# Kernel tuning notes

Hardware: AMD Instinct MI355X
Metric: run time of the kernel (lower is better)

Reference implementation:

```python
import jax, jax.numpy as jnp
import numpy as np

N_NODES = 50000
N_EDGES = 400000
D_IN = 256
D_OUT = 256
DROPOUT_P = 0.1


def setup_inputs() -> dict:
    key = jax.random.key(0)
    k_feat, k_w, k_src, k_dst = jax.random.split(key, 4)
    feat = jax.random.normal(k_feat, (N_NODES, D_IN), dtype=jnp.float32)
    # Glorot-ish init for the GraphConv weight
    W = jax.random.normal(k_w, (D_IN, D_OUT), dtype=jnp.float32) * (1.0 / np.sqrt(D_IN))
    b = jnp.zeros((D_OUT,), dtype=jnp.float32)
    src = jax.random.randint(k_src, (N_EDGES,), 0, N_NODES, dtype=jnp.int32)
    dst = jax.random.randint(k_dst, (N_EDGES,), 0, N_NODES, dtype=jnp.int32)
    return {"feat": feat, "W": W, "b": b, "src": src, "dst": dst}


def reference(feat, W, b, src, dst):
    # Degrees from the edge list (DGL GraphConv norm='both'):
    # src is normalized by out-degree, dst by in-degree; clamp to >= 1.
    ones = jnp.ones((src.shape[0],), dtype=feat.dtype)
    deg_out = jnp.clip(jax.ops.segment_sum(ones, src, num_segments=N_NODES), 1.0)
    deg_in = jnp.clip(jax.ops.segment_sum(ones, dst, num_segments=N_NODES), 1.0)

    # Pre-normalize, project, then gather-scatter aggregate (mult W first,
    # mathematically identical to DGL's ordering since dims are equal).
    x = feat * jax.lax.rsqrt(deg_out)[:, None]          # [N, D_in]
    x = x @ W                                            # [N, D_out]
    agg = jax.ops.segment_sum(x[src], dst, num_segments=N_NODES)  # [N, D_out]
    h = agg * jax.lax.rsqrt(deg_in)[:, None] + b

    # Activation + dropout (training-mode, deterministic key)
    h = jax.nn.relu(h)
    keep = jax.random.bernoulli(jax.random.key(42), 1.0 - DROPOUT_P, h.shape)
    h = jnp.where(keep, h / (1.0 - DROPOUT_P), 0.0)
    return h
```

## Files before the change

kernel.cpp:

```cpp
#include <hip/hip_runtime.h>
#include <stdint.h>

#define N_NODES 50000
#define N_EDGES 400000
#define DDIM 256
#define MASK_WORDS 400000
#define EDGE_CAP 64

typedef __attribute__((ext_vector_type(8))) short bf16x8;
typedef __attribute__((ext_vector_type(4))) float f32x4;

__device__ __forceinline__ uint32_t rotl32(uint32_t x, uint32_t r) {
  return (x << r) | (x >> (32u - r));
}

__device__ __forceinline__ uint32_t threefry_draw_0_42(uint32_t x0, uint32_t x1) {
  const uint32_t k0 = 0u, k1 = 42u;
  const uint32_t k2 = k0 ^ k1 ^ 0x1BD11BDAu;
  x0 += k0;
  x1 += k1;
#define TF_ROUND(r)          \
  {                          \
    x0 += x1;                \
    x1 = rotl32(x1, r);      \
    x1 ^= x0;                \
  }
  TF_ROUND(13) TF_ROUND(15) TF_ROUND(26) TF_ROUND(6)
  x0 += k1; x1 += k2 + 1u;
  TF_ROUND(17) TF_ROUND(29) TF_ROUND(16) TF_ROUND(24)
  x0 += k2; x1 += k0 + 2u;
  TF_ROUND(13) TF_ROUND(15) TF_ROUND(26) TF_ROUND(6)
  x0 += k0; x1 += k1 + 3u;
  TF_ROUND(17) TF_ROUND(29) TF_ROUND(16) TF_ROUND(24)
  x0 += k1; x1 += k2 + 4u;
  TF_ROUND(13) TF_ROUND(15) TF_ROUND(26) TF_ROUND(6)
  x0 += k2; x1 += k0 + 5u;
#undef TF_ROUND
  return x0 ^ x1;
}

__device__ __forceinline__ uint16_t bf16_rne(float x) {
  uint32_t u = __float_as_uint(x);
  u += 0x7FFFu + ((u >> 16) & 1u);
  return (uint16_t)(u >> 16);
}

__device__ __forceinline__ float bf16_to_f32(uint16_t x) {
  return __uint_as_float(((uint32_t)x) << 16);
}

__global__ __launch_bounds__(256) void setup_kernel(
    const float* __restrict__ W, uint16_t* __restrict__ Wt,
    int4* __restrict__ zero_base) {
  const int bid = blockIdx.x;
  if (bid < 98) {
    const int t = bid * 256 + threadIdx.x;
    if (t < 25000) zero_base[t] = make_int4(0, 0, 0, 0);
  } else {
    const int t = (bid - 98) * 256 + threadIdx.x;
    const int n = t >> 6;
    const int k4 = (t & 63) << 2;
    ushort4 p;
    p.x = bf16_rne(W[(size_t)(k4 + 0) * DDIM + n]);
    p.y = bf16_rne(W[(size_t)(k4 + 1) * DDIM + n]);
    p.z = bf16_rne(W[(size_t)(k4 + 2) * DDIM + n]);
    p.w = bf16_rne(W[(size_t)(k4 + 3) * DDIM + n]);
    *(ushort4*)(Wt + (size_t)n * DDIM + k4) = p;
  }
}

__global__ __launch_bounds__(256) void degree_fill_kernel(
    const int* __restrict__ src, const int* __restrict__ dst,
    int* __restrict__ deg_out, int* __restrict__ deg_in,
    int* __restrict__ esrc) {
  const int e = blockIdx.x * 256 + threadIdx.x;
  if (e < N_EDGES) {
    const int s = src[e];
    const int d = dst[e];
    atomicAdd(&deg_out[s], 1);
    const int pos = atomicAdd(&deg_in[d], 1);
    if (pos < EDGE_CAP) esrc[(d << 6) + pos] = s;
  }
}

__global__ __launch_bounds__(256) void fconv_kernel(
    const float* __restrict__ feat, const int* __restrict__ deg_out,
    uint16_t* __restrict__ featb) {
  const int t = blockIdx.x * 256 + threadIdx.x;
  const size_t base = (size_t)t * 8;
  const int row = t >> 5;
  const float sc = rsqrtf(fmaxf((float)deg_out[row], 1.0f));
  const float4 a = *(const float4*)(feat + base);
  const float4 b = *(const float4*)(feat + base + 4);
  ushort4 lo, hi;
  lo.x = bf16_rne(a.x * sc); lo.y = bf16_rne(a.y * sc);
  lo.z = bf16_rne(a.z * sc); lo.w = bf16_rne(a.w * sc);
  hi.x = bf16_rne(b.x * sc); hi.y = bf16_rne(b.y * sc);
  hi.z = bf16_rne(b.z * sc); hi.w = bf16_rne(b.w * sc);
  *(ushort4*)(featb + base) = lo;
  *(ushort4*)(featb + base + 4) = hi;
}

__global__ __launch_bounds__(256) void gather_mask_kernel(
    const uint16_t* __restrict__ featb, const int* __restrict__ deg_in,
    const int* __restrict__ esrc, uint16_t* __restrict__ agg,
    uint32_t* __restrict__ mask) {
  const int bid = blockIdx.x;
  const int tid = threadIdx.x;

  if ((bid % 9) == 8) {
    const uint32_t t = (uint32_t)(bid / 9) * 256u + (uint32_t)tid;
    if (t < MASK_WORDS) {
      const uint32_t base = t * 32u;
      uint32_t w = 0u;
#pragma unroll
      for (uint32_t b = 0; b < 32u; ++b) {
        const uint32_t bits = threefry_draw_0_42(0u, base + b);
        w |= ((bits >> 9) < 7549747u) ? (1u << b) : 0u;
      }
      mask[t] = w;
    }
    return;
  }

  const int g = (bid / 9) * 8 + (bid % 9);
  const int n = g * 4 + (tid >> 6);
  if (n >= N_NODES) return;
  const int lane = tid & 63;
  const int beg = n << 6;
  const int fin = beg + min(deg_in[n], EDGE_CAP);
  const size_t off = (size_t)(lane << 2);
  float4 a0 = {0.f, 0.f, 0.f, 0.f}, a1 = a0, a2 = a0, a3 = a0;
  int j = beg;
  for (; j + 4 <= fin; j += 4) {
    const int s0 = esrc[j + 0];
    const int s1 = esrc[j + 1];
    const int s2 = esrc[j + 2];
    const int s3 = esrc[j + 3];
    const ushort4 q0 = *(const ushort4*)(featb + (size_t)s0 * DDIM + off);
    const ushort4 q1 = *(const ushort4*)(featb + (size_t)s1 * DDIM + off);
    const ushort4 q2 = *(const ushort4*)(featb + (size_t)s2 * DDIM + off);
    const ushort4 q3 = *(const ushort4*)(featb + (size_t)s3 * DDIM + off);
    a0.x += bf16_to_f32(q0.x); a0.y += bf16_to_f32(q0.y);
    a0.z += bf16_to_f32(q0.z); a0.w += bf16_to_f32(q0.w);
    a1.x += bf16_to_f32(q1.x); a1.y += bf16_to_f32(q1.y);
    a1.z += bf16_to_f32(q1.z); a1.w += bf16_to_f32(q1.w);
    a2.x += bf16_to_f32(q2.x); a2.y += bf16_to_f32(q2.y);
    a2.z += bf16_to_f32(q2.z); a2.w += bf16_to_f32(q2.w);
    a3.x += bf16_to_f32(q3.x); a3.y += bf16_to_f32(q3.y);
    a3.z += bf16_to_f32(q3.z); a3.w += bf16_to_f32(q3.w);
  }
  for (; j < fin; ++j) {
    const int s = esrc[j];
    const ushort4 q = *(const ushort4*)(featb + (size_t)s * DDIM + off);
    a0.x += bf16_to_f32(q.x); a0.y += bf16_to_f32(q.y);
    a0.z += bf16_to_f32(q.z); a0.w += bf16_to_f32(q.w);
  }
  float4 acc;
  acc.x = (a0.x + a1.x) + (a2.x + a3.x);
  acc.y = (a0.y + a1.y) + (a2.y + a3.y);
  acc.z = (a0.z + a1.z) + (a2.z + a3.z);
  acc.w = (a0.w + a1.w) + (a2.w + a3.w);
  ushort4 p;
  p.x = bf16_rne(acc.x);
  p.y = bf16_rne(acc.y);
  p.z = bf16_rne(acc.z);
  p.w = bf16_rne(acc.w);
  *(ushort4*)(agg + (size_t)n * DDIM + off) = p;
}

#define APAD 280
__global__ __launch_bounds__(256, 4) void gemm_mfma_kernel(
    const uint16_t* __restrict__ agg, const uint16_t* __restrict__ Wt,
    const float* __restrict__ bias, const int* __restrict__ deg_in,
    const uint32_t* __restrict__ mask, float* __restrict__ out) {
  __shared__ short As[64 * APAD];
  __shared__ float sdeg[64];
  __shared__ float sbias[256];

  const int tid = threadIdx.x;
  const int r0 = blockIdx.x * 64;
  const int lane = tid & 63;
  const int seg = lane >> 4;
  const int l15 = lane & 15;
  const int wc = tid >> 6;

  sbias[tid] = bias[tid];
  if (tid < 64) {
    const int r = r0 + tid;
    sdeg[tid] = (r < N_NODES) ? rsqrtf(fmaxf((float)deg_in[r], 1.0f)) : 0.0f;
  }

  {
    const uint16_t* ap = agg + (size_t)r0 * DDIM;
#pragma unroll
    for (int it = 0; it < 8; ++it) {
      const int c = tid + 256 * it;
      const int row = c >> 5;
      const int k8 = (c & 31) << 3;
      int4 v = make_int4(0, 0, 0, 0);
      if (r0 + row < N_NODES) v = *(const int4*)(ap + (size_t)row * DDIM + k8);
      *(int4*)&As[row * APAD + k8] = v;
    }
  }
  __syncthreads();

  const uint16_t* wt_base = Wt + (size_t)(wc * 64 + l15) * DDIM + seg * 8;

  f32x4 acc[4][4] = {};
#pragma unroll
  for (int kkI = 0; kkI < 8; ++kkI) {
    const int kk = kkI * 32;
    bf16x8 a[4], b[4];
#pragma unroll
    for (int m = 0; m < 4; ++m)
      a[m] = *(const bf16x8*)&As[(m * 16 + l15) * APAD + kk + seg * 8];
#pragma unroll
    for (int n = 0; n < 4; ++n)
      b[n] = *(const bf16x8*)(wt_base + n * 16 * DDIM + kk);
#pragma unroll
    for (int m = 0; m < 4; ++m)
#pragma unroll
      for (int n = 0; n < 4; ++n)
        acc[m][n] = __builtin_amdgcn_mfma_f32_16x16x32_bf16(a[m], b[n], acc[m][n], 0, 0, 0);
  }

  constexpr float INV09 = 1.0f / 0.9f;
#pragma unroll
  for (int m = 0; m < 4; ++m) {
#pragma unroll
    for (int r = 0; r < 4; ++r) {
      const int lrow = m * 16 + seg * 4 + r;
      const int row = r0 + lrow;
      if (row >= N_NODES) continue;
      const float s = sdeg[lrow];
      const uint32_t w0 = mask[row * 8 + wc * 2];
      const uint32_t w1 = mask[row * 8 + wc * 2 + 1];
#pragma unroll
      for (int n = 0; n < 4; ++n) {
        const int col = wc * 64 + n * 16 + l15;
        float v = fmaxf(acc[m][n][r] * s + sbias[col], 0.0f);
        const uint32_t w = (n < 2) ? w0 : w1;
        const uint32_t bit = (uint32_t)((n & 1) * 16 + l15);
        out[(size_t)row * DDIM + col] = ((w >> bit) & 1u) ? v * INV09 : 0.0f;
      }
    }
  }
}

extern "C" void kernel_launch(void* const* d_in, const int* in_sizes, int n_in,
                              void* d_out, int out_size, void* d_ws, size_t ws_size,
                              hipStream_t stream) {
  const float* feat = (const float*)d_in[0];
  const float* W = (const float*)d_in[1];
  const float* bias = (const float*)d_in[2];
  const int* src = (const int*)d_in[3];
  const int* dst = (const int*)d_in[4];
  float* out = (float*)d_out;

  char* ws = (char*)d_ws;
  int* deg_out = (int*)(ws + 0);
  int* deg_in = (int*)(ws + 200000);
  int* esrc = (int*)(ws + 400000);
  uint16_t* Wt = (uint16_t*)(ws + 13200000);
  uint16_t* agg = (uint16_t*)(ws + 13331072);
  uint32_t* mask = (uint32_t*)(ws + 38931072);
  uint16_t* featb = (uint16_t*)d_out;

  setup_kernel<<<162, 256, 0, stream>>>(W, Wt, (int4*)d_ws);
  degree_fill_kernel<<<(N_EDGES + 255) / 256, 256, 0, stream>>>(src, dst, deg_out, deg_in, esrc);
  fconv_kernel<<<6250, 256, 0, stream>>>(feat, deg_out, featb);
  gather_mask_kernel<<<14067, 256, 0, stream>>>(featb, deg_in, esrc, agg, mask);
  gemm_mfma_kernel<<<(N_NODES + 63) / 64, 256, 0, stream>>>(agg, Wt, bias, deg_in, mask, out);
}
```

Before: 138.2 us.

## Fuse neighbor gather into GEMM kernel and move mask generation to degree kernel

```diff
diff --git a/kernel.cpp b/kernel.cpp
--- a/kernel.cpp
+++ b/kernel.cpp
@@ -6,6 +6,8 @@
 #define DDIM 256
 #define MASK_WORDS 400000
 #define EDGE_CAP 64
+#define DEG_BLOCKS 1563
+#define MASK_BLOCKS 1563
 
 typedef __attribute__((ext_vector_type(8))) short bf16x8;
 typedef __attribute__((ext_vector_type(4))) float f32x4;
@@ -69,17 +71,32 @@
   }
 }
 
-__global__ __launch_bounds__(256) void degree_fill_kernel(
+__global__ __launch_bounds__(256) void degree_fill_mask_kernel(
     const int* __restrict__ src, const int* __restrict__ dst,
     int* __restrict__ deg_out, int* __restrict__ deg_in,
-    int* __restrict__ esrc) {
-  const int e = blockIdx.x * 256 + threadIdx.x;
-  if (e < N_EDGES) {
-    const int s = src[e];
-    const int d = dst[e];
-    atomicAdd(&deg_out[s], 1);
-    const int pos = atomicAdd(&deg_in[d], 1);
-    if (pos < EDGE_CAP) esrc[(d << 6) + pos] = s;
+    int* __restrict__ esrc, uint32_t* __restrict__ mask) {
+  const int bid = blockIdx.x;
+  if (bid < DEG_BLOCKS) {
+    const int e = bid * 256 + threadIdx.x;
+    if (e < N_EDGES) {
+      const int s = src[e];
+      const int d = dst[e];
+      atomicAdd(&deg_out[s], 1);
+      const int pos = atomicAdd(&deg_in[d], 1);
+      if (pos < EDGE_CAP) esrc[(d << 6) + pos] = s;
+    }
+  } else {
+    const uint32_t t = (uint32_t)(bid - DEG_BLOCKS) * 256u + (uint32_t)threadIdx.x;
+    if (t < MASK_WORDS) {
+      const uint32_t base = t * 32u;
+      uint32_t w = 0u;
+#pragma unroll
+      for (uint32_t b = 0; b < 32u; ++b) {
+        const uint32_t bits = threefry_draw_0_42(0u, base + b);
+        w |= ((bits >> 9) < 7549747u) ? (1u << b) : 0u;
+      }
+      mask[t] = w;
+    }
   }
 }
 
@@ -101,79 +118,12 @@
   *(ushort4*)(featb + base + 4) = hi;
 }
 
-__global__ __launch_bounds__(256) void gather_mask_kernel(
+#define APAD 280
+__global__ __launch_bounds__(256, 4) void gather_gemm_kernel(
     const uint16_t* __restrict__ featb, const int* __restrict__ deg_in,
-    const int* __restrict__ esrc, uint16_t* __restrict__ agg,
-    uint32_t* __restrict__ mask) {
-  const int bid = blockIdx.x;
-  const int tid = threadIdx.x;
-
-  if ((bid % 9) == 8) {
-    const uint32_t t = (uint32_t)(bid / 9) * 256u + (uint32_t)tid;
-    if (t < MASK_WORDS) {
-      const uint32_t base = t * 32u;
-      uint32_t w = 0u;
-#pragma unroll
-      for (uint32_t b = 0; b < 32u; ++b) {
-        const uint32_t bits = threefry_draw_0_42(0u, base + b);
-        w |= ((bits >> 9) < 7549747u) ? (1u << b) : 0u;
-      }
-      mask[t] = w;
-    }
-    return;
-  }
-
-  const int g = (bid / 9) * 8 + (bid % 9);
-  const int n = g * 4 + (tid >> 6);
-  if (n >= N_NODES) return;
-  const int lane = tid & 63;
-  const int beg = n << 6;
-  const int fin = beg + min(deg_in[n], EDGE_CAP);
-  const size_t off = (size_t)(lane << 2);
-  float4 a0 = {0.f, 0.f, 0.f, 0.f}, a1 = a0, a2 = a0, a3 = a0;
-  int j = beg;
-  for (; j + 4 <= fin; j += 4) {
-    const int s0 = esrc[j + 0];
-    const int s1 = esrc[j + 1];
-    const int s2 = esrc[j + 2];
-    const int s3 = esrc[j + 3];
-    const ushort4 q0 = *(const ushort4*)(featb + (size_t)s0 * DDIM + off);
-    const ushort4 q1 = *(const ushort4*)(featb + (size_t)s1 * DDIM + off);
-    const ushort4 q2 = *(const ushort4*)(featb + (size_t)s2 * DDIM + off);
-    const ushort4 q3 = *(const ushort4*)(featb + (size_t)s3 * DDIM + off);
-    a0.x += bf16_to_f32(q0.x); a0.y += bf16_to_f32(q0.y);
-    a0.z += bf16_to_f32(q0.z); a0.w += bf16_to_f32(q0.w);
-    a1.x += bf16_to_f32(q1.x); a1.y += bf16_to_f32(q1.y);
-    a1.z += bf16_to_f32(q1.z); a1.w += bf16_to_f32(q1.w);
-    a2.x += bf16_to_f32(q2.x); a2.y += bf16_to_f32(q2.y);
-    a2.z += bf16_to_f32(q2.z); a2.w += bf16_to_f32(q2.w);
-    a3.x += bf16_to_f32(q3.x); a3.y += bf16_to_f32(q3.y);
-    a3.z += bf16_to_f32(q3.z); a3.w += bf16_to_f32(q3.w);
-  }
-  for (; j < fin; ++j) {
-    const int s = esrc[j];
-    const ushort4 q = *(const ushort4*)(featb + (size_t)s * DDIM + off);
-    a0.x += bf16_to_f32(q.x); a0.y += bf16_to_f32(q.y);
-    a0.z += bf16_to_f32(q.z); a0.w += bf16_to_f32(q.w);
-  }
-  float4 acc;
-  acc.x = (a0.x + a1.x) + (a2.x + a3.x);
-  acc.y = (a0.y + a1.y) + (a2.y + a3.y);
-  acc.z = (a0.z + a1.z) + (a2.z + a3.z);
-  acc.w = (a0.w + a1.w) + (a2.w + a3.w);
-  ushort4 p;
-  p.x = bf16_rne(acc.x);
-  p.y = bf16_rne(acc.y);
-  p.z = bf16_rne(acc.z);
-  p.w = bf16_rne(acc.w);
-  *(ushort4*)(agg + (size_t)n * DDIM + off) = p;
-}
-
-#define APAD 280
-__global__ __launch_bounds__(256, 4) void gemm_mfma_kernel(
-    const uint16_t* __restrict__ agg, const uint16_t* __restrict__ Wt,
-    const float* __restrict__ bias, const int* __restrict__ deg_in,
-    const uint32_t* __restrict__ mask, float* __restrict__ out) {
+    const int* __restrict__ esrc, const uint16_t* __restrict__ Wt,
+    const float* __restrict__ bias, const uint32_t* __restrict__ mask,
+    float* __restrict__ out) {
   __shared__ short As[64 * APAD];
   __shared__ float sdeg[64];
   __shared__ float sbias[256];
@@ -181,9 +131,9 @@
   const int tid = threadIdx.x;
   const int r0 = blockIdx.x * 64;
   const int lane = tid & 63;
+  const int wv = tid >> 6;
   const int seg = lane >> 4;
   const int l15 = lane & 15;
-  const int wc = tid >> 6;
 
   sbias[tid] = bias[tid];
   if (tid < 64) {
@@ -191,21 +141,50 @@
     sdeg[tid] = (r < N_NODES) ? rsqrtf(fmaxf((float)deg_in[r], 1.0f)) : 0.0f;
   }
 
-  {
-    const uint16_t* ap = agg + (size_t)r0 * DDIM;
-#pragma unroll
-    for (int it = 0; it < 8; ++it) {
-      const int c = tid + 256 * it;
-      const int row = c >> 5;
-      const int k8 = (c & 31) << 3;
-      int4 v = make_int4(0, 0, 0, 0);
-      if (r0 + row < N_NODES) v = *(const int4*)(ap + (size_t)row * DDIM + k8);
-      *(int4*)&As[row * APAD + k8] = v;
-    }
+  const size_t off = (size_t)(lane << 2);
+  for (int i = 0; i < 16; ++i) {
+    const int lrow = wv * 16 + i;
+    const int n = r0 + lrow;
+    float4 a0 = {0.f, 0.f, 0.f, 0.f}, a1 = a0, a2 = a0, a3 = a0;
+    if (n < N_NODES) {
+      const int beg = n << 6;
+      const int fin = beg + min(deg_in[n], EDGE_CAP);
+      int j = beg;
+      for (; j + 4 <= fin; j += 4) {
+        const int s0 = esrc[j + 0];
+        const int s1 = esrc[j + 1];
+        const int s2 = esrc[j + 2];
+        const int s3 = esrc[j + 3];
+        const ushort4 q0 = *(const ushort4*)(featb + (size_t)s0 * DDIM + off);
+        const ushort4 q1 = *(const ushort4*)(featb + (size_t)s1 * DDIM + off);
+        const ushort4 q2 = *(const ushort4*)(featb + (size_t)s2 * DDIM + off);
+        const ushort4 q3 = *(const ushort4*)(featb + (size_t)s3 * DDIM + off);
+        a0.x += bf16_to_f32(q0.x); a0.y += bf16_to_f32(q0.y);
+        a0.z += bf16_to_f32(q0.z); a0.w += bf16_to_f32(q0.w);
+        a1.x += bf16_to_f32(q1.x); a1.y += bf16_to_f32(q1.y);
+        a1.z += bf16_to_f32(q1.z); a1.w += bf16_to_f32(q1.w);
+        a2.x += bf16_to_f32(q2.x); a2.y += bf16_to_f32(q2.y);
+        a2.z += bf16_to_f32(q2.z); a2.w += bf16_to_f32(q2.w);
+        a3.x += bf16_to_f32(q3.x); a3.y += bf16_to_f32(q3.y);
+        a3.z += bf16_to_f32(q3.z); a3.w += bf16_to_f32(q3.w);
+      }
+      for (; j < fin; ++j) {
+        const int s = esrc[j];
+        const ushort4 q = *(const ushort4*)(featb + (size_t)s * DDIM + off);
+        a0.x += bf16_to_f32(q.x); a0.y += bf16_to_f32(q.y);
+        a0.z += bf16_to_f32(q.z); a0.w += bf16_to_f32(q.w);
+      }
+    }
+    ushort4 p;
+    p.x = bf16_rne((a0.x + a1.x) + (a2.x + a3.x));
+    p.y = bf16_rne((a0.y + a1.y) + (a2.y + a3.y));
+    p.z = bf16_rne((a0.z + a1.z) + (a2.z + a3.z));
+    p.w = bf16_rne((a0.w + a1.w) + (a2.w + a3.w));
+    *(ushort4*)&As[lrow * APAD + (lane << 2)] = p;
   }
   __syncthreads();
 
-  const uint16_t* wt_base = Wt + (size_t)(wc * 64 + l15) * DDIM + seg * 8;
+  const uint16_t* wt_base = Wt + (size_t)(wv * 64 + l15) * DDIM + seg * 8;
 
   f32x4 acc[4][4] = {};
 #pragma unroll
@@ -234,11 +213,11 @@
       const int row = r0 + lrow;
       if (row >= N_NODES) continue;
       const float s = sdeg[lrow];
-      const uint32_t w0 = mask[row * 8 + wc * 2];
-      const uint32_t w1 = mask[row * 8 + wc * 2 + 1];
+      const uint32_t w0 = mask[row * 8 + wv * 2];
+      const uint32_t w1 = mask[row * 8 + wv * 2 + 1];
 #pragma unroll
       for (int n = 0; n < 4; ++n) {
-        const int col = wc * 64 + n * 16 + l15;
+        const int col = wv * 64 + n * 16 + l15;
         float v = fmaxf(acc[m][n][r] * s + sbias[col], 0.0f);
         const uint32_t w = (n < 2) ? w0 : w1;
         const uint32_t bit = (uint32_t)((n & 1) * 16 + l15);
@@ -263,13 +242,13 @@
   int* deg_in = (int*)(ws + 200000);
   int* esrc = (int*)(ws + 400000);
   uint16_t* Wt = (uint16_t*)(ws + 13200000);
-  uint16_t* agg = (uint16_t*)(ws + 13331072);
+  uint16_t* featb = (uint16_t*)(ws + 13331072);
   uint32_t* mask = (uint32_t*)(ws + 38931072);
-  uint16_t* featb = (uint16_t*)d_out;
 
   setup_kernel<<<162, 256, 0, stream>>>(W, Wt, (int4*)d_ws);
-  degree_fill_kernel<<<(N_EDGES + 255) / 256, 256, 0, stream>>>(src, dst, deg_out, deg_in, esrc);
+  degree_fill_mask_kernel<<<DEG_BLOCKS + MASK_BLOCKS, 256, 0, stream>>>(
+      src, dst, deg_out, deg_in, esrc, mask);
   fconv_kernel<<<6250, 256, 0, stream>>>(feat, deg_out, featb);
-  gather_mask_kernel<<<14067, 256, 0, stream>>>(featb, deg_in, esrc, agg, mask);
-  gemm_mfma_kernel<<<(N_NODES + 63) / 64, 256, 0, stream>>>(agg, Wt, bias, deg_in, mask, out);
-}
+  gather_gemm_kernel<<<(N_NODES + 63) / 64, 256, 0, stream>>>(
+      featb, deg_in, esrc, Wt, bias, mask, out);
+}
```

New measurement: 150.2 us. 1.09x slower.

## Move dropout mask into degree kernel and widen gather loads to 16 bytes

Applied to the files above, without the earlier changes.

```diff
diff --git a/kernel.cpp b/kernel.cpp
--- a/kernel.cpp
+++ b/kernel.cpp
@@ -6,6 +6,7 @@
 #define DDIM 256
 #define MASK_WORDS 400000
 #define EDGE_CAP 64
+#define DEG_BLOCKS 1563
 
 typedef __attribute__((ext_vector_type(8))) short bf16x8;
 typedef __attribute__((ext_vector_type(4))) float f32x4;
@@ -69,17 +70,32 @@
   }
 }
 
-__global__ __launch_bounds__(256) void degree_fill_kernel(
+__global__ __launch_bounds__(256) void degree_fill_mask_kernel(
     const int* __restrict__ src, const int* __restrict__ dst,
     int* __restrict__ deg_out, int* __restrict__ deg_in,
-    int* __restrict__ esrc) {
-  const int e = blockIdx.x * 256 + threadIdx.x;
-  if (e < N_EDGES) {
-    const int s = src[e];
-    const int d = dst[e];
-    atomicAdd(&deg_out[s], 1);
-    const int pos = atomicAdd(&deg_in[d], 1);
-    if (pos < EDGE_CAP) esrc[(d << 6) + pos] = s;
+    int* __restrict__ esrc, uint32_t* __restrict__ mask) {
+  const int bid = blockIdx.x;
+  if (bid < DEG_BLOCKS) {
+    const int e = bid * 256 + threadIdx.x;
+    if (e < N_EDGES) {
+      const int s = src[e];
+      const int d = dst[e];
+      atomicAdd(&deg_out[s], 1);
+      const int pos = atomicAdd(&deg_in[d], 1);
+      if (pos < EDGE_CAP) esrc[(d << 6) + pos] = s;
+    }
+  } else {
+    const uint32_t t = (uint32_t)(bid - DEG_BLOCKS) * 256u + (uint32_t)threadIdx.x;
+    if (t < MASK_WORDS) {
+      const uint32_t base = t * 32u;
+      uint32_t w = 0u;
+#pragma unroll
+      for (uint32_t b = 0; b < 32u; ++b) {
+        const uint32_t bits = threefry_draw_0_42(0u, base + b);
+        w |= ((bits >> 9) < 7549747u) ? (1u << b) : 0u;
+      }
+      mask[t] = w;
+    }
   }
 }
 
@@ -101,72 +117,68 @@
   *(ushort4*)(featb + base + 4) = hi;
 }
 
-__global__ __launch_bounds__(256) void gather_mask_kernel(
+__device__ __forceinline__ void acc8(float* a, uint4 q) {
+  a[0] += __uint_as_float(q.x << 16);
+  a[1] += __uint_as_float(q.x & 0xFFFF0000u);
+  a[2] += __uint_as_float(q.y << 16);
+  a[3] += __uint_as_float(q.y & 0xFFFF0000u);
+  a[4] += __uint_as_float(q.z << 16);
+  a[5] += __uint_as_float(q.z & 0xFFFF0000u);
+  a[6] += __uint_as_float(q.w << 16);
+  a[7] += __uint_as_float(q.w & 0xFFFF0000u);
+}
+
+__global__ __launch_bounds__(256) void gather_kernel(
     const uint16_t* __restrict__ featb, const int* __restrict__ deg_in,
-    const int* __restrict__ esrc, uint16_t* __restrict__ agg,
-    uint32_t* __restrict__ mask) {
-  const int bid = blockIdx.x;
-  const int tid = threadIdx.x;
-
-  if ((bid % 9) == 8) {
-    const uint32_t t = (uint32_t)(bid / 9) * 256u + (uint32_t)tid;
-    if (t < MASK_WORDS) {
-      const uint32_t base = t * 32u;
-      uint32_t w = 0u;
-#pragma unroll
-      for (uint32_t b = 0; b < 32u; ++b) {
-        const uint32_t bits = threefry_draw_0_42(0u, base + b);
-        w |= ((bits >> 9) < 7549747u) ? (1u << b) : 0u;
-      }
-      mask[t] = w;
-    }
-    return;
-  }
-
-  const int g = (bid / 9) * 8 + (bid % 9);
-  const int n = g * 4 + (tid >> 6);
+    const int* __restrict__ esrc, uint16_t* __restrict__ agg) {
+  const int n = blockIdx.x * 4 + (threadIdx.x >> 6);
   if (n >= N_NODES) return;
-  const int lane = tid & 63;
+  const int lane = threadIdx.x & 63;
+  const int eh = lane >> 5;
+  const int l32 = lane & 31;
+  const size_t coff = (size_t)(l32 << 3);
   const int beg = n << 6;
-  const int fin = beg + min(deg_in[n], EDGE_CAP);
-  const size_t off = (size_t)(lane << 2);
-  float4 a0 = {0.f, 0.f, 0.f, 0.f}, a1 = a0, a2 = a0, a3 = a0;
-  int j = beg;
-  for (; j + 4 <= fin; j += 4) {
-    const int s0 = esrc[j + 0];
-    const int s1 = esrc[j + 1];
-    const int s2 = esrc[j + 2];
-    const int s3 = esrc[j + 3];
-    const ushort4 q0 = *(const ushort4*)(featb + (size_t)s0 * DDIM + off);
-    const ushort4 q1 = *(const ushort4*)(featb + (size_t)s1 * DDIM + off);
-    const ushort4 q2 = *(const ushort4*)(featb + (size_t)s2 * DDIM + off);
-    const ushort4 q3 = *(const ushort4*)(featb + (size_t)s3 * DDIM + off);
-    a0.x += bf16_to_f32(q0.x); a0.y += bf16_to_f32(q0.y);
-    a0.z += bf16_to_f32(q0.z); a0.w += bf16_to_f32(q0.w);
-    a1.x += bf16_to_f32(q1.x); a1.y += bf16_to_f32(q1.y);
-    a1.z += bf16_to_f32(q1.z); a1.w += bf16_to_f32(q1.w);
-    a2.x += bf16_to_f32(q2.x); a2.y += bf16_to_f32(q2.y);
-    a2.z += bf16_to_f32(q2.z); a2.w += bf16_to_f32(q2.w);
-    a3.x += bf16_to_f32(q3.x); a3.y += bf16_to_f32(q3.y);
-    a3.z += bf16_to_f32(q3.z); a3.w += bf16_to_f32(q3.w);
-  }
-  for (; j < fin; ++j) {
-    const int s = esrc[j];
-    const ushort4 q = *(const ushort4*)(featb + (size_t)s * DDIM + off);
-    a0.x += bf16_to_f32(q.x); a0.y += bf16_to_f32(q.y);
-    a0.z += bf16_to_f32(q.z); a0.w += bf16_to_f32(q.w);
-  }
-  float4 acc;
-  acc.x = (a0.x + a1.x) + (a2.x + a3.x);
-  acc.y = (a0.y + a1.y) + (a2.y + a3.y);
-  acc.z = (a0.z + a1.z) + (a2.z + a3.z);
-  acc.w = (a0.w + a1.w) + (a2.w + a3.w);
-  ushort4 p;
-  p.x = bf16_rne(acc.x);
-  p.y = bf16_rne(acc.y);
-  p.z = bf16_rne(acc.z);
-  p.w = bf16_rne(acc.w);
-  *(ushort4*)(agg + (size_t)n * DDIM + off) = p;
+  const int cnt = min(deg_in[n], EDGE_CAP);
+
+  float a0[8] = {}, a1[8] = {}, a2[8] = {}, a3[8] = {};
+  int j = 0;
+  for (; j + 8 <= cnt; j += 8) {
+    const int s0 = esrc[beg + j + 0 + eh];
+    const int s1 = esrc[beg + j + 2 + eh];
+    const int s2 = esrc[beg + j + 4 + eh];
+    const int s3 = esrc[beg + j + 6 + eh];
+    const uint4 q0 = *(const uint4*)(featb + (size_t)s0 * DDIM + coff);
+    const uint4 q1 = *(const uint4*)(featb + (size_t)s1 * DDIM + coff);
+    const uint4 q2 = *(const uint4*)(featb + (size_t)s2 * DDIM + coff);
+    const uint4 q3 = *(const uint4*)(featb + (size_t)s3 * DDIM + coff);
+    acc8(a0, q0);
+    acc8(a1, q1);
+    acc8(a2, q2);
+    acc8(a3, q3);
+  }
+  for (; j + 2 <= cnt; j += 2) {
+    const int s = esrc[beg + j + eh];
+    const uint4 q = *(const uint4*)(featb + (size_t)s * DDIM + coff);
+    acc8(a0, q);
+  }
+  if (j < cnt && eh == 0) {
+    const int s = esrc[beg + j];
+    const uint4 q = *(const uint4*)(featb + (size_t)s * DDIM + coff);
+    acc8(a0, q);
+  }
+
+  uint4 p;
+  uint32_t pk[4];
+#pragma unroll
+  for (int k = 0; k < 8; k += 2) {
+    float lo = (a0[k] + a1[k]) + (a2[k] + a3[k]);
+    float hi = (a0[k + 1] + a1[k + 1]) + (a2[k + 1] + a3[k + 1]);
+    lo += __shfl_xor(lo, 32);
+    hi += __shfl_xor(hi, 32);
+    pk[k >> 1] = (uint32_t)bf16_rne(lo) | ((uint32_t)bf16_rne(hi) << 16);
+  }
+  p.x = pk[0]; p.y = pk[1]; p.z = pk[2]; p.w = pk[3];
+  if (eh == 0) *(uint4*)(agg + (size_t)n * DDIM + coff) = p;
 }
 
 #define APAD 280
@@ -263,13 +275,14 @@
   int* deg_in = (int*)(ws + 200000);
   int* esrc = (int*)(ws + 400000);
   uint16_t* Wt = (uint16_t*)(ws + 13200000);
-  uint16_t* agg = (uint16_t*)(ws + 13331072);
+  uint16_t* featb = (uint16_t*)(ws + 13331072);
   uint32_t* mask = (uint32_t*)(ws + 38931072);
-  uint16_t* featb = (uint16_t*)d_out;
+  uint16_t* agg = (uint16_t*)(ws + 40531072);
 
   setup_kernel<<<162, 256, 0, stream>>>(W, Wt, (int4*)d_ws);
-  degree_fill_kernel<<<(N_EDGES + 255) / 256, 256, 0, stream>>>(src, dst, deg_out, deg_in, esrc);
+  degree_fill_mask_kernel<<<DEG_BLOCKS + 1563, 256, 0, stream>>>(
+      src, dst, deg_out, deg_in, esrc, mask);
   fconv_kernel<<<6250, 256, 0, stream>>>(feat, deg_out, featb);
-  gather_mask_kernel<<<14067, 256, 0, stream>>>(featb, deg_in, esrc, agg, mask);
+  gather_kernel<<<(N_NODES + 3) / 4, 256, 0, stream>>>(featb, deg_in, esrc, agg);
   gemm_mfma_kernel<<<(N_NODES + 63) / 64, 256, 0, stream>>>(agg, Wt, bias, deg_in, mask, out);
 }
```

Result: slower. 147.0 us (+6.3%).
